# Optimization experiments

Hardware: AMD Instinct MI355X
Metric: run time of the kernel (lower is better)

The kernel has to match this reference:

```python
import jax, jax.numpy as jnp
import numpy as np
from jax import lax

T, B, E = 1500, 32, 512   # encoder frames, batch, encoded_size
H = 512                   # hidden_size
NC = 31                   # num_classes + 1 (EOS = 30)
LTXT = 100                # max text len before EOS column


def setup_inputs() -> dict:
    key = jax.random.key(0)
    ks = jax.random.split(key, 24)
    sE = 1.0 / np.sqrt(E); sH = 1.0 / np.sqrt(H); sIn = 1.0 / np.sqrt(H + E)
    inp = {
        'encoded': jax.random.normal(ks[0], (T, B, E), jnp.float32),
        'encoded_lens': jax.random.randint(ks[1], (B,), 1, T + 1),
        'texts': jax.random.randint(ks[2], (B, LTXT), 0, 30).astype(jnp.int32),
        'text_lens': jax.random.randint(ks[3], (B,), 1, LTXT + 1),
        # attention params
        'W_enc': jax.random.normal(ks[4], (H, E), jnp.float32) * sE,
        'b_enc': jax.random.normal(ks[5], (H,), jnp.float32) * sE,
        'W_rec': jax.random.normal(ks[6], (H, H), jnp.float32) * sH,
        'w_score': jax.random.normal(ks[7], (H,), jnp.float32) * sH,
        'b_score': jax.random.normal(ks[8], (), jnp.float32) * sH,
        # embedding
        'emb': jax.random.normal(ks[9], (NC, H), jnp.float32),
        # GRU layer 0 (input = H + E)
        'W_ih0': jax.random.normal(ks[10], (3 * H, H + E), jnp.float32) * sIn,
        'W_hh0': jax.random.normal(ks[11], (3 * H, H), jnp.float32) * sH,
        'b_ih0': jax.random.normal(ks[12], (3 * H,), jnp.float32) * sH,
        'b_hh0': jax.random.normal(ks[13], (3 * H,), jnp.float32) * sH,
        # GRU layer 1 (input = H)
        'W_ih1': jax.random.normal(ks[14], (3 * H, H), jnp.float32) * sH,
        'W_hh1': jax.random.normal(ks[15], (3 * H, H), jnp.float32) * sH,
        'b_ih1': jax.random.normal(ks[16], (3 * H,), jnp.float32) * sH,
        'b_hh1': jax.random.normal(ks[17], (3 * H,), jnp.float32) * sH,
        # output projection
        'W_out': jax.random.normal(ks[18], (NC, H), jnp.float32) * sH,
        'b_out': jax.random.normal(ks[19], (NC,), jnp.float32) * sH,
        # learned rnn zero state (n_layers, 1, H)
        'h0': jnp.zeros((2, 1, H), jnp.float32),
    }
    return inp


def _gru_cell(x, h, W_ih, W_hh, b_ih, b_hh):
    gi = x @ W_ih.T + b_ih
    gh = h @ W_hh.T + b_hh
    i_r, i_z, i_n = jnp.split(gi, 3, axis=-1)
    h_r, h_z, h_n = jnp.split(gh, 3, axis=-1)
    r = jax.nn.sigmoid(i_r + h_r)
    z = jax.nn.sigmoid(i_z + h_z)
    n = jnp.tanh(i_n + r * h_n)
    return (1.0 - z) * n + z * h


def reference(encoded, encoded_lens, texts, text_lens, W_enc, b_enc, W_rec,
              w_score, b_score, emb, W_ih0, W_hh0, b_ih0, b_hh0, W_ih1,
              W_hh1, b_ih1, b_hh1, W_out, b_out, h0):
    Tt, Bb, Ee = encoded.shape
    Hh = W_rec.shape[0]
    EOS = emb.shape[0] - 1
    # append zero column, then write EOS at text_lens position
    texts2 = jnp.concatenate([texts, jnp.zeros((Bb, 1), texts.dtype)], axis=1)
    texts2 = texts2.at[jnp.arange(Bb), text_lens].set(EOS)
    L = texts2.shape[1]
    embedded = emb[texts2.T]                               # (L, B, H)
    enc_contrib = encoded @ W_enc.T + b_enc                # (T, B, H)
    mask = (jnp.arange(Tt)[:, None] < encoded_lens[None, :]).astype(encoded.dtype)
    mask = (mask - 1.0) * 100000.0                         # (T, B)
    rnn0 = jnp.broadcast_to(h0, (2, Bb, Hh))

    def step(carry, target):
        rnn_state, inputs = carry
        rec = rnn_state[0] @ W_rec.T                       # (B, H)
        scores = jnp.tanh(enc_contrib + rec[None]) @ w_score + b_score  # (T, B)
        att = jax.nn.softmax(scores + mask, axis=0)        # (T, B)
        context = jnp.einsum('tb,tbe->be', att, encoded)   # (B, E)
        x = jnp.concatenate([inputs, context], axis=1)     # (B, H+E)
        h0n = _gru_cell(x, rnn_state[0], W_ih0, W_hh0, b_ih0, b_hh0)
        h1n = _gru_cell(h0n, rnn_state[1], W_ih1, W_hh1, b_ih1, b_hh1)
        return (jnp.stack([h0n, h1n]), target), h1n

    init = (rnn0, jnp.zeros((Bb, Hh), encoded.dtype))
    _, outputs = lax.scan(step, init, embedded)            # (L, B, H)
    logits = outputs @ W_out.T + b_out                     # (L, B, NC)
    logits = jnp.transpose(logits, (1, 0, 2)).reshape(Bb * L, -1)
    labels = texts2.reshape(-1)
    logp = jax.nn.log_softmax(logits, axis=-1)
    nll = -jnp.take_along_axis(logp, labels[:, None].astype(jnp.int32), axis=1)[:, 0]
    valid = (labels != 0).astype(logits.dtype)
    loss = jnp.sum(nll * valid) / jnp.maximum(jnp.sum(valid), 1.0)
    return loss
```

## Files before the change

kernel.cpp:

```cpp
#include <hip/hip_runtime.h>
#include <hip/hip_cooperative_groups.h>
#include <stdint.h>

#define T_FRAMES 1500
#define B_BATCH  32
#define E_DIM    512
#define H_DIM    512
#define NCLS     31
#define L_STEPS  101
#define EOS_TOK  30
#define NBLK     256
#define NTHR     1024
#define NSLICE   8

typedef unsigned short ushort_t;
typedef ushort_t ushort8_t __attribute__((ext_vector_type(8)));
typedef unsigned char uchar8_t __attribute__((ext_vector_type(8)));

__device__ __forceinline__ float bf2f(ushort_t u) {
    union { unsigned int i; float f; } v; v.i = ((unsigned int)u) << 16; return v.f;
}
__device__ __forceinline__ ushort_t f2bf(float f) {
    union { float f; unsigned int i; } v; v.f = f;
    unsigned int r = v.i + 0x7FFFu + ((v.i >> 16) & 1u);
    return (ushort_t)(r >> 16);
}
__device__ __forceinline__ float fp8tof(unsigned int u) {
    unsigned int e = (u >> 3) & 15u, m = u & 7u, sg = (u >> 7) & 1u;
    union { unsigned int i; float f; } v;
    v.i = (sg << 31) | ((e + 120u) << 23) | (m << 20);
    float sub = (float)(int)m * 0.001953125f;
    sub = sg ? -sub : sub;
    return e ? v.f : sub;
}
__device__ __forceinline__ unsigned char f2fp8(float x) {
    unsigned char sg = (x < 0.f) ? 0x80 : 0;
    float a = fabsf(x);
    if (!(a == a)) return (unsigned char)(sg | 0x7E);
    if (a >= 448.f) return (unsigned char)(sg | 0x7E);
    if (a < 0.015625f) {
        int m = (int)rintf(a * 512.f);
        if (m >= 8) return (unsigned char)(sg | 0x08);
        return (unsigned char)(sg | m);
    }
    union { float f; unsigned int i; } v; v.f = a;
    unsigned int r = v.i + 0x7FFFFu + ((v.i >> 20) & 1u);
    unsigned int e = (r >> 23) - 127u + 7u;
    unsigned int m = (r >> 20) & 7u;
    if (e > 15u || (e == 15u && m == 7u)) { e = 15u; m = 6u; }
    return (unsigned char)(sg | (e << 3) | m);
}
__device__ __forceinline__ float wave_sum(float v) {
    #pragma unroll
    for (int o = 32; o > 0; o >>= 1) v += __shfl_xor(v, o, 64);
    return v;
}
template<int N>
__device__ __forceinline__ void wave_sum_n(float* v) {
    #pragma unroll
    for (int o = 32; o > 0; o >>= 1) {
        #pragma unroll
        for (int i = 0; i < N; ++i) v[i] += __shfl_xor(v[i], o, 64);
    }
}
__device__ __forceinline__ float tanh_f(float x) {
    float e = __expf(2.0f * x);
    return 1.0f - 2.0f * __builtin_amdgcn_rcpf(e + 1.0f);
}
__device__ __forceinline__ float sigmoid_f(float x) {
    return __builtin_amdgcn_rcpf(1.0f + __expf(-x));
}

__device__ __forceinline__ float ld_byp(const float* p) {
    return __hip_atomic_load(p, __ATOMIC_RELAXED, __HIP_MEMORY_SCOPE_AGENT);
}
__device__ __forceinline__ void st_byp(float* p, float v) {
    __hip_atomic_store(p, v, __ATOMIC_RELAXED, __HIP_MEMORY_SCOPE_AGENT);
}

__device__ __forceinline__ void ffbarrier(int* flags, int base, int s, int k, int tid) {
    __syncthreads();
    if (tid == 0)
        __hip_atomic_store(&flags[(base + s) * 32], k,
                           __ATOMIC_RELAXED, __HIP_MEMORY_SCOPE_AGENT);
    if (tid < NSLICE) {
        while (__hip_atomic_load(&flags[(base + tid) * 32],
                                 __ATOMIC_RELAXED, __HIP_MEMORY_SCOPE_AGENT) < k)
            __builtin_amdgcn_s_sleep(1);
    }
    __syncthreads();
    asm volatile("" ::: "memory");
}

__global__ __launch_bounds__(256) void init_kernel(
    const int* __restrict__ texts, const int* __restrict__ text_lens,
    const float* __restrict__ h0p,
    int* __restrict__ texts2, float* __restrict__ h0buf, float* __restrict__ h1buf,
    float* __restrict__ acc, int* __restrict__ flags)
{
    int idx = blockIdx.x * 256 + threadIdx.x;
    if (idx < 2) acc[idx] = 0.f;
    if (idx < B_BATCH * NSLICE * 32) flags[idx] = 0;
    if (idx < B_BATCH * L_STEPS) {
        int b = idx / L_STEPS, j = idx % L_STEPS;
        int v = (j < 100) ? texts[b * 100 + j] : 0;
        if (j == text_lens[b]) v = EOS_TOK;
        texts2[idx] = v;
    }
    for (int i = idx; i < B_BATCH * H_DIM; i += gridDim.x * 256) {
        h0buf[i] = h0p[i & (H_DIM - 1)];
        h1buf[i] = h0p[H_DIM + (i & (H_DIM - 1))];
    }
}

__global__ __launch_bounds__(256) void cvt_kernel(const float* __restrict__ in,
                                                  ushort_t* __restrict__ out, int n) {
    int i = (blockIdx.x * 256 + threadIdx.x) * 8;
    if (i >= n) return;
    float4 a = *(const float4*)(in + i);
    float4 b = *(const float4*)(in + i + 4);
    ushort8_t o;
    o[0] = f2bf(a.x); o[1] = f2bf(a.y); o[2] = f2bf(a.z); o[3] = f2bf(a.w);
    o[4] = f2bf(b.x); o[5] = f2bf(b.y); o[6] = f2bf(b.z); o[7] = f2bf(b.w);
    *(ushort8_t*)(out + i) = o;
}

__global__ __launch_bounds__(64) void cvt_fp8_transpose_kernel(const float* __restrict__ in,
                                                               unsigned char* __restrict__ out) {
    int row = blockIdx.x;
    int t = row >> 5, b = row & 31;
    int k = threadIdx.x * 8;
    const float* ip = in + (size_t)row * E_DIM + k;
    float4 a = *(const float4*)(ip);
    float4 c = *(const float4*)(ip + 4);
    float vals[8] = {a.x, a.y, a.z, a.w, c.x, c.y, c.z, c.w};
    uchar8_t o;
    #pragma unroll
    for (int j = 0; j < 8; ++j) o[j] = f2fp8(vals[j]);
    *(uchar8_t*)(out + ((size_t)b * T_FRAMES + t) * E_DIM + k) = o;
}

#define GTM 128
#define GTN 128
#define GTK 32
#define GLDA (GTM + 4)

__global__ __launch_bounds__(256) void enc_gemm_kernel(
    const float* __restrict__ A, const float* __restrict__ W,
    const float* __restrict__ bias, ushort_t* __restrict__ C)
{
    __shared__ float As[GTK][GLDA];
    __shared__ float Bs[GTK][GLDA];
    const int m0 = blockIdx.y * GTM;
    const int n0 = blockIdx.x * GTN;
    const int tid = threadIdx.x;
    const int tx = tid & 15, ty = tid >> 4;
    const int lr = tid >> 3;
    const int lc = (tid & 7) << 2;
    float acc[8][8] = {};
    for (int k0 = 0; k0 < E_DIM; k0 += GTK) {
        #pragma unroll
        for (int p = 0; p < 4; ++p) {
            float4 a = *(const float4*)(A + (size_t)(m0 + lr + 32 * p) * E_DIM + k0 + lc);
            As[lc + 0][lr + 32 * p] = a.x; As[lc + 1][lr + 32 * p] = a.y;
            As[lc + 2][lr + 32 * p] = a.z; As[lc + 3][lr + 32 * p] = a.w;
            float4 b = *(const float4*)(W + (size_t)(n0 + lr + 32 * p) * E_DIM + k0 + lc);
            Bs[lc + 0][lr + 32 * p] = b.x; Bs[lc + 1][lr + 32 * p] = b.y;
            Bs[lc + 2][lr + 32 * p] = b.z; Bs[lc + 3][lr + 32 * p] = b.w;
        }
        __syncthreads();
        #pragma unroll
        for (int k = 0; k < GTK; ++k) {
            float av[8], bv[8];
            *(float4*)&av[0] = *(const float4*)&As[k][ty * 8];
            *(float4*)&av[4] = *(const float4*)&As[k][ty * 8 + 4];
            *(float4*)&bv[0] = *(const float4*)&Bs[k][tx * 8];
            *(float4*)&bv[4] = *(const float4*)&Bs[k][tx * 8 + 4];
            #pragma unroll
            for (int i = 0; i < 8; ++i)
                #pragma unroll
                for (int j = 0; j < 8; ++j)
                    acc[i][j] = fmaf(av[i], bv[j], acc[i][j]);
        }
        __syncthreads();
    }
    const float* bp = bias + n0 + tx * 8;
    #pragma unroll
    for (int i = 0; i < 8; ++i) {
        int m = m0 + ty * 8 + i;
        int b = m & 31, t = m >> 5;
        ushort8_t o;
        #pragma unroll
        for (int j = 0; j < 8; ++j) o[j] = f2bf(acc[i][j] + bp[j]);
        *(ushort8_t*)(C + ((size_t)b * T_FRAMES + t) * H_DIM + n0 + tx * 8) = o;
    }
}

struct Params {
    const float* encoded; const int* lens; const float* emb;
    const float* w_score; const float* b_score;
    const float* b_ih0; const float* b_hh0; const float* b_ih1; const float* b_hh1;
    const ushort_t* ec; const unsigned char* encF8;
    const ushort_t* Wrec; const ushort_t* Wih0; const ushort_t* Whh0;
    const ushort_t* Wih1; const ushort_t* Whh1;
    float* rec; float* ctxPart; float* denomPart;
    float* h0a; float* h0b; float* h1a; float* h1b;
    float* outputs; const int* texts2; int* flags;
    int useEncB;
};

__global__ __launch_bounds__(NTHR, 1) void decoder_kernel(Params p) {
    const int tid = threadIdx.x;
    const int bid = blockIdx.x;
    const int lane = tid & 63;
    const int wsub = tid >> 6;
    const int b = bid >> 3;
    const int s = bid & 7;
    const int fbase = b * NSLICE;
    __shared__ float sctx[16][E_DIM];
    __shared__ float sred[16];
    float* sA = &sctx[0][0];
    float* sB = &sctx[1][0];

    {
        const float* xp = p.h0a + b * H_DIM + lane * 8;
        float x8[8];
        *(float4*)&x8[0] = *(const float4*)(xp);
        *(float4*)&x8[4] = *(const float4*)(xp + 4);
        #pragma unroll
        for (int i = 0; i < 4; ++i) {
            int h = s * 64 + wsub * 4 + i;
            ushort8_t w8 = *(const ushort8_t*)(p.Wrec + (size_t)h * H_DIM + lane * 8);
            float v = 0.f;
            #pragma unroll
            for (int j = 0; j < 8; ++j) v = fmaf(x8[j], bf2f(w8[j]), v);
            v = wave_sum(v);
            if (lane == 0) st_byp(&p.rec[b * H_DIM + h], v);
        }
    }
    ffbarrier(p.flags, fbase, s, 1, tid);

    const int len = p.lens[b];
    for (int l = 0; l < L_STEPS; ++l) {
        float* h0cur = (l & 1) ? p.h0b : p.h0a;
        float* h0nxt = (l & 1) ? p.h0a : p.h0b;
        float* h1cur = (l & 1) ? p.h1b : p.h1a;
        float* h1nxt = (l & 1) ? p.h1a : p.h1b;

        {
            for (int i = tid; i < H_DIM; i += NTHR)
                sA[i] = ld_byp(&p.rec[b * H_DIM + i]);
            __syncthreads();
            float rec8[8], w8[8];
            #pragma unroll
            for (int j = 0; j < 8; ++j) rec8[j] = sA[lane * 8 + j];
            const float* wp = p.w_score + lane * 8;
            *(float4*)&w8[0] = *(const float4*)(wp);
            *(float4*)&w8[4] = *(const float4*)(wp + 4);
            float bsc = p.b_score[0];
            __syncthreads();
            float acc8[8] = {0.f,0.f,0.f,0.f,0.f,0.f,0.f,0.f};
            float dsum = 0.f;
            const int gw = wsub * NSLICE + s;
            if (p.useEncB) {
                const ushort_t* ecb = p.ec + (size_t)b * T_FRAMES * H_DIM + lane * 8;
                const unsigned char* efb = p.encF8 + (size_t)b * T_FRAMES * E_DIM + lane * 8;
                for (int t = gw; t < len; t += 256) {
                    int t2 = t + 128;
                    bool has2 = t2 < len;
                    int t2c = has2 ? t2 : t;
                    ushort8_t e8a = *(const ushort8_t*)(ecb + (size_t)t   * H_DIM);
                    ushort8_t e8b = *(const ushort8_t*)(ecb + (size_t)t2c * H_DIM);
                    uchar8_t v8a = *(const uchar8_t*)(efb + (size_t)t   * E_DIM);
                    uchar8_t v8b = *(const uchar8_t*)(efb + (size_t)t2c * E_DIM);
                    float ss[2] = {0.f, 0.f};
                    #pragma unroll
                    for (int j = 0; j < 8; ++j) {
                        ss[0] = fmaf(tanh_f(bf2f(e8a[j]) + rec8[j]), w8[j], ss[0]);
                        ss[1] = fmaf(tanh_f(bf2f(e8b[j]) + rec8[j]), w8[j], ss[1]);
                    }
                    wave_sum_n<2>(ss);
                    float pv0 = __expf(ss[0] + bsc);
                    float pv1 = has2 ? __expf(ss[1] + bsc) : 0.f;
                    dsum += pv0 + pv1;
                    #pragma unroll
                    for (int j = 0; j < 8; ++j)
                        acc8[j] += pv0 * fp8tof(v8a[j]) + pv1 * fp8tof(v8b[j]);
                }
            } else {
                const ushort_t* ecb = p.ec + (size_t)b * T_FRAMES * H_DIM + lane * 8;
                for (int t = gw; t < len; t += 128) {
                    ushort8_t e8 = *(const ushort8_t*)(ecb + (size_t)t * H_DIM);
                    float ss = 0.f;
                    #pragma unroll
                    for (int j = 0; j < 8; ++j)
                        ss = fmaf(tanh_f(bf2f(e8[j]) + rec8[j]), w8[j], ss);
                    ss = wave_sum(ss) + bsc;
                    float pv = __expf(ss);
                    dsum += pv;
                    const float* vp = p.encoded + ((size_t)t * B_BATCH + b) * E_DIM + lane * 8;
                    float v8[8];
                    *(float4*)&v8[0] = *(const float4*)(vp);
                    *(float4*)&v8[4] = *(const float4*)(vp + 4);
                    #pragma unroll
                    for (int j = 0; j < 8; ++j)
                        acc8[j] = fmaf(pv, v8[j], acc8[j]);
                }
            }
            *(float4*)&sctx[wsub][lane * 8]     = *(float4*)&acc8[0];
            *(float4*)&sctx[wsub][lane * 8 + 4] = *(float4*)&acc8[4];
            if (lane == 0) sred[wsub] = dsum;
            __syncthreads();
            if (tid < E_DIM) {
                float csum = 0.f;
                #pragma unroll
                for (int w = 0; w < 16; ++w) csum += sctx[w][tid];
                st_byp(&p.ctxPart[((size_t)b * NSLICE + s) * E_DIM + tid], csum);
            }
            if (tid == 0) {
                float d = 0.f;
                #pragma unroll
                for (int w = 0; w < 16; ++w) d += sred[w];
                st_byp(&p.denomPart[b * NSLICE + s], d);
            }
        }
        ffbarrier(p.flags, fbase, s, 3 * l + 2, tid);

        {
            if (tid < E_DIM) {
                float c = 0.f;
                #pragma unroll
                for (int s2 = 0; s2 < NSLICE; ++s2)
                    c += ld_byp(&p.ctxPart[((size_t)b * NSLICE + s2) * E_DIM + tid]);
                sA[tid] = c;
                sB[tid] = ld_byp(&h0cur[b * H_DIM + tid]);
            } else if (tid < E_DIM + NSLICE) {
                sred[tid - E_DIM] = ld_byp(&p.denomPart[b * NSLICE + (tid - E_DIM)]);
            }
            __syncthreads();
            float den = sred[0] + sred[1] + sred[2] + sred[3]
                      + sred[4] + sred[5] + sred[6] + sred[7];
            float inv = __builtin_amdgcn_rcpf(den);
            int token = (l > 0) ? p.texts2[b * L_STEPS + l - 1] : -1;
            float x16[16];
            int k0 = lane * 16;
            if (k0 < H_DIM) {
                if (token >= 0) {
                    const float* ep = p.emb + (size_t)token * H_DIM + k0;
                    #pragma unroll
                    for (int q = 0; q < 4; ++q)
                        *(float4*)&x16[q * 4] = *(const float4*)(ep + q * 4);
                } else {
                    #pragma unroll
                    for (int j = 0; j < 16; ++j) x16[j] = 0.f;
                }
            } else {
                #pragma unroll
                for (int j = 0; j < 16; ++j) x16[j] = sA[k0 - H_DIM + j] * inv;
            }
            float h8[8];
            #pragma unroll
            for (int j = 0; j < 8; ++j) h8[j] = sB[lane * 8 + j];
            const int IN = H_DIM + E_DIM;
            #pragma unroll
            for (int i = 0; i < 4; ++i) {
                int h = s * 64 + wsub * 4 + i;
                float v[6] = {0.f,0.f,0.f,0.f,0.f,0.f};
                #pragma unroll
                for (int g = 0; g < 3; ++g) {
                    const ushort_t* r = p.Wih0 + (size_t)(g * H_DIM + h) * IN + k0;
                    ushort8_t a = *(const ushort8_t*)(r);
                    ushort8_t c = *(const ushort8_t*)(r + 8);
                    #pragma unroll
                    for (int j = 0; j < 8; ++j) {
                        v[g] = fmaf(x16[j], bf2f(a[j]), v[g]);
                        v[g] = fmaf(x16[8 + j], bf2f(c[j]), v[g]);
                    }
                }
                #pragma unroll
                for (int g = 0; g < 3; ++g) {
                    const ushort_t* r = p.Whh0 + (size_t)(g * H_DIM + h) * H_DIM + lane * 8;
                    ushort8_t a = *(const ushort8_t*)(r);
                    #pragma unroll
                    for (int j = 0; j < 8; ++j)
                        v[3 + g] = fmaf(h8[j], bf2f(a[j]), v[3 + g]);
                }
                wave_sum_n<6>(v);
                if (lane == 0) {
                    float r = sigmoid_f(v[0] + p.b_ih0[h] + v[3] + p.b_hh0[h]);
                    float z = sigmoid_f(v[1] + p.b_ih0[H_DIM + h] + v[4] + p.b_hh0[H_DIM + h]);
                    float n = tanh_f(v[2] + p.b_ih0[2 * H_DIM + h] + r * (v[5] + p.b_hh0[2 * H_DIM + h]));
                    float hv = sB[h];
                    st_byp(&h0nxt[b * H_DIM + h], (1.f - z) * n + z * hv);
                }
            }
        }
        ffbarrier(p.flags, fbase, s, 3 * l + 3, tid);

        {
            if (tid < E_DIM) {
                sA[tid] = ld_byp(&h0nxt[b * H_DIM + tid]);
                sB[tid] = ld_byp(&h1cur[b * H_DIM + tid]);
            }
            __syncthreads();
            float x8[8], g8[8];
            #pragma unroll
            for (int j = 0; j < 8; ++j) { x8[j] = sA[lane * 8 + j]; g8[j] = sB[lane * 8 + j]; }
            #pragma unroll
            for (int i = 0; i < 4; ++i) {
                int h = s * 64 + wsub * 4 + i;
                float v[7] = {0.f,0.f,0.f,0.f,0.f,0.f,0.f};
                #pragma unroll
                for (int g = 0; g < 3; ++g) {
                    const ushort_t* r1 = p.Wih1 + (size_t)(g * H_DIM + h) * H_DIM + lane * 8;
                    ushort8_t a = *(const ushort8_t*)(r1);
                    const ushort_t* r2 = p.Whh1 + (size_t)(g * H_DIM + h) * H_DIM + lane * 8;
                    ushort8_t c = *(const ushort8_t*)(r2);
                    #pragma unroll
                    for (int j = 0; j < 8; ++j) {
                        v[g]     = fmaf(x8[j], bf2f(a[j]), v[g]);
                        v[3 + g] = fmaf(g8[j], bf2f(c[j]), v[3 + g]);
                    }
                }
                {
                    const ushort_t* r = p.Wrec + (size_t)h * H_DIM + lane * 8;
                    ushort8_t a = *(const ushort8_t*)(r);
                    #pragma unroll
                    for (int j = 0; j < 8; ++j)
                        v[6] = fmaf(x8[j], bf2f(a[j]), v[6]);
                }
                wave_sum_n<7>(v);
                if (lane == 0) {
                    float r = sigmoid_f(v[0] + p.b_ih1[h] + v[3] + p.b_hh1[h]);
                    float z = sigmoid_f(v[1] + p.b_ih1[H_DIM + h] + v[4] + p.b_hh1[H_DIM + h]);
                    float n = tanh_f(v[2] + p.b_ih1[2 * H_DIM + h] + r * (v[5] + p.b_hh1[2 * H_DIM + h]));
                    float hv = sB[h];
                    float out = (1.f - z) * n + z * hv;
                    st_byp(&h1nxt[b * H_DIM + h], out);
                    p.outputs[((size_t)l * B_BATCH + b) * H_DIM + h] = out;
                    st_byp(&p.rec[b * H_DIM + h], v[6]);
                }
            }
        }
        ffbarrier(p.flags, fbase, s, 3 * l + 4, tid);
    }
}

__global__ __launch_bounds__(256) void loss_kernel(
    const float* __restrict__ outputs, const int* __restrict__ texts2,
    const float* __restrict__ W_out, const float* __restrict__ b_out,
    float* __restrict__ acc)
{
    int wid = threadIdx.x >> 6, lane = threadIdx.x & 63;
    int gw = blockIdx.x * 4 + wid;
    int nw = gridDim.x * 4;
    float lsum = 0.f, lcnt = 0.f;
    for (int r = gw; r < B_BATCH * L_STEPS; r += nw) {
        int b = r / L_STEPS, l = r % L_STEPS;
        int label = texts2[r];
        const float* orow = outputs + ((size_t)l * B_BATCH + b) * H_DIM;
        int k = lane * 8;
        float o8[8];
        *(float4*)&o8[0] = *(const float4*)(orow + k);
        *(float4*)&o8[4] = *(const float4*)(orow + k + 4);
        float m = -1e30f, se = 0.f, ll = 0.f;
        for (int c = 0; c < NCLS; ++c) {
            const float* wrow = W_out + (size_t)c * H_DIM + k;
            float p = 0.f;
            #pragma unroll
            for (int j = 0; j < 8; ++j) p = fmaf(o8[j], wrow[j], p);
            float logit = wave_sum(p) + b_out[c];
            if (c == label) ll = logit;
            if (logit > m) { se = se * expf(m - logit) + 1.f; m = logit; }
            else           { se += expf(logit - m); }
        }
        float lse = m + logf(se);
        if (label != 0) { lsum += lse - ll; lcnt += 1.f; }
    }
    if (lane == 0) { atomicAdd(&acc[0], lsum); atomicAdd(&acc[1], lcnt); }
}

__global__ void finalize_kernel(const float* __restrict__ acc, float* __restrict__ out) {
    out[0] = acc[0] / fmaxf(acc[1], 1.0f);
}

static inline size_t align256(size_t x) { return (x + 255) & ~(size_t)255; }

extern "C" void kernel_launch(void* const* d_in, const int* in_sizes, int n_in,
                              void* d_out, int out_size, void* d_ws, size_t ws_size,
                              hipStream_t stream) {
    (void)in_sizes; (void)n_in; (void)out_size;
    const float* encoded      = (const float*)d_in[0];
    const int*   encoded_lens = (const int*)d_in[1];
    const int*   texts        = (const int*)d_in[2];
    const int*   text_lens    = (const int*)d_in[3];
    const float* W_enc        = (const float*)d_in[4];
    const float* b_enc        = (const float*)d_in[5];
    const float* W_rec        = (const float*)d_in[6];
    const float* w_score      = (const float*)d_in[7];
    const float* b_score      = (const float*)d_in[8];
    const float* emb          = (const float*)d_in[9];
    const float* W_ih0        = (const float*)d_in[10];
    const float* W_hh0        = (const float*)d_in[11];
    const float* b_ih0        = (const float*)d_in[12];
    const float* b_hh0        = (const float*)d_in[13];
    const float* W_ih1        = (const float*)d_in[14];
    const float* W_hh1        = (const float*)d_in[15];
    const float* b_ih1        = (const float*)d_in[16];
    const float* b_hh1        = (const float*)d_in[17];
    const float* W_out        = (const float*)d_in[18];
    const float* b_out        = (const float*)d_in[19];
    const float* h0p          = (const float*)d_in[20];

    char* ws = (char*)d_ws;
    size_t off = 0;
    ushort_t* ec     = (ushort_t*)(ws + off); off = align256(off + (size_t)T_FRAMES * B_BATCH * H_DIM * 2);
    ushort_t* Wrecb  = (ushort_t*)(ws + off); off = align256(off + (size_t)H_DIM * H_DIM * 2);
    ushort_t* Wih0b  = (ushort_t*)(ws + off); off = align256(off + (size_t)3 * H_DIM * (H_DIM + E_DIM) * 2);
    ushort_t* Whh0b  = (ushort_t*)(ws + off); off = align256(off + (size_t)3 * H_DIM * H_DIM * 2);
    ushort_t* Wih1b  = (ushort_t*)(ws + off); off = align256(off + (size_t)3 * H_DIM * H_DIM * 2);
    ushort_t* Whh1b  = (ushort_t*)(ws + off); off = align256(off + (size_t)3 * H_DIM * H_DIM * 2);
    float* rec       = (float*)(ws + off); off = align256(off + (size_t)B_BATCH * H_DIM * 4);
    float* ctxPart   = (float*)(ws + off); off = align256(off + (size_t)B_BATCH * NSLICE * E_DIM * 4);
    float* denomPart = (float*)(ws + off); off = align256(off + (size_t)B_BATCH * NSLICE * 4);
    float* h0a       = (float*)(ws + off); off = align256(off + (size_t)B_BATCH * H_DIM * 4);
    float* h0b       = (float*)(ws + off); off = align256(off + (size_t)B_BATCH * H_DIM * 4);
    float* h1a       = (float*)(ws + off); off = align256(off + (size_t)B_BATCH * H_DIM * 4);
    float* h1b       = (float*)(ws + off); off = align256(off + (size_t)B_BATCH * H_DIM * 4);
    float* outputs   = (float*)(ws + off); off = align256(off + (size_t)L_STEPS * B_BATCH * H_DIM * 4);
    int*   texts2    = (int*)(ws + off); off = align256(off + (size_t)B_BATCH * L_STEPS * 4);
    float* acc       = (float*)(ws + off); off = align256(off + 256);
    int*   flags     = (int*)(ws + off); off = align256(off + (size_t)B_BATCH * NSLICE * 32 * 4);
    size_t encF8_off = off;
    size_t encF8_bytes = (size_t)T_FRAMES * B_BATCH * E_DIM;
    int useEncB = (encF8_off + encF8_bytes <= ws_size) ? 1 : 0;
    unsigned char* encF8 = (unsigned char*)(ws + encF8_off);

    init_kernel<<<64, 256, 0, stream>>>(texts, text_lens, h0p, texts2, h0a, h1a, acc, flags);
    cvt_kernel<<<(H_DIM * H_DIM) / (256 * 8), 256, 0, stream>>>(W_rec, Wrecb, H_DIM * H_DIM);
    cvt_kernel<<<(3 * H_DIM * (H_DIM + E_DIM)) / (256 * 8), 256, 0, stream>>>(W_ih0, Wih0b, 3 * H_DIM * (H_DIM + E_DIM));
    cvt_kernel<<<(3 * H_DIM * H_DIM) / (256 * 8), 256, 0, stream>>>(W_hh0, Whh0b, 3 * H_DIM * H_DIM);
    cvt_kernel<<<(3 * H_DIM * H_DIM) / (256 * 8), 256, 0, stream>>>(W_ih1, Wih1b, 3 * H_DIM * H_DIM);
    cvt_kernel<<<(3 * H_DIM * H_DIM) / (256 * 8), 256, 0, stream>>>(W_hh1, Whh1b, 3 * H_DIM * H_DIM);
    if (useEncB) {
        cvt_fp8_transpose_kernel<<<T_FRAMES * B_BATCH, 64, 0, stream>>>(encoded, encF8);
    }
    enc_gemm_kernel<<<dim3(H_DIM / GTN, (T_FRAMES * B_BATCH) / GTM), 256, 0, stream>>>(
        encoded, W_enc, b_enc, ec);

    Params prm;
    prm.encoded = encoded; prm.lens = encoded_lens; prm.emb = emb;
    prm.w_score = w_score; prm.b_score = b_score;
    prm.b_ih0 = b_ih0; prm.b_hh0 = b_hh0; prm.b_ih1 = b_ih1; prm.b_hh1 = b_hh1;
    prm.ec = ec; prm.encF8 = encF8;
    prm.Wrec = Wrecb; prm.Wih0 = Wih0b; prm.Whh0 = Whh0b; prm.Wih1 = Wih1b; prm.Whh1 = Whh1b;
    prm.rec = rec; prm.ctxPart = ctxPart; prm.denomPart = denomPart;
    prm.h0a = h0a; prm.h0b = h0b; prm.h1a = h1a; prm.h1b = h1b;
    prm.outputs = outputs; prm.texts2 = texts2; prm.flags = flags;
    prm.useEncB = useEncB;

    void* args[] = { &prm };
    hipLaunchCooperativeKernel((const void*)decoder_kernel, dim3(NBLK), dim3(NTHR),
                               args, 0, stream);

    loss_kernel<<<64, 256, 0, stream>>>(outputs, texts2, W_out, b_out, acc);
    finalize_kernel<<<1, 1, 0, stream>>>(acc, (float*)d_out);
}
```

Measured before the change: 8.736 ms.

## Interleave fp8 enc-projection and values into fused layout; double decoder blocks

Stores the encoder projection in fp8 instead of bf16 and interleaves it with the fp8 encoded values into one 1024-byte row per frame. Each lane now does a single 16-byte load that covers both the score and context operands. The decoder grid doubles to 512 blocks with 16 slices per batch, so each block handles half the hidden rows and a smaller stride of frames. This halves the traffic of the per-step attention scan but adds fp8 rounding error to the scores. It also relies on the cooperative launch fitting 512 blocks of 1024 threads, with launch bounds raised to 8.

```diff
diff --git a/kernel.cpp b/kernel.cpp
--- a/kernel.cpp
+++ b/kernel.cpp
@@ -9,13 +9,14 @@
 #define NCLS     31
 #define L_STEPS  101
 #define EOS_TOK  30
-#define NBLK     256
+#define NBLK     512
 #define NTHR     1024
-#define NSLICE   8
+#define NSLICE   16
 
 typedef unsigned short ushort_t;
 typedef ushort_t ushort8_t __attribute__((ext_vector_type(8)));
 typedef unsigned char uchar8_t __attribute__((ext_vector_type(8)));
+typedef unsigned char uchar16_t __attribute__((ext_vector_type(16)));
 
 __device__ __forceinline__ float bf2f(ushort_t u) {
     union { unsigned int i; float f; } v; v.i = ((unsigned int)u) << 16; return v.f;
@@ -125,8 +126,8 @@
     *(ushort8_t*)(out + i) = o;
 }
 
-__global__ __launch_bounds__(64) void cvt_fp8_transpose_kernel(const float* __restrict__ in,
-                                                               unsigned char* __restrict__ out) {
+__global__ __launch_bounds__(64) void cvt_fused_enc_kernel(const float* __restrict__ in,
+                                                           unsigned char* __restrict__ fused) {
     int row = blockIdx.x;
     int t = row >> 5, b = row & 31;
     int k = threadIdx.x * 8;
@@ -137,7 +138,7 @@
     uchar8_t o;
     #pragma unroll
     for (int j = 0; j < 8; ++j) o[j] = f2fp8(vals[j]);
-    *(uchar8_t*)(out + ((size_t)b * T_FRAMES + t) * E_DIM + k) = o;
+    *(uchar8_t*)(fused + ((size_t)b * T_FRAMES + t) * 1024 + threadIdx.x * 16 + 8) = o;
 }
 
 #define GTM 128
@@ -147,7 +148,7 @@
 
 __global__ __launch_bounds__(256) void enc_gemm_kernel(
     const float* __restrict__ A, const float* __restrict__ W,
-    const float* __restrict__ bias, ushort_t* __restrict__ C)
+    const float* __restrict__ bias, unsigned char* __restrict__ fused)
 {
     __shared__ float As[GTK][GLDA];
     __shared__ float Bs[GTK][GLDA];
@@ -189,33 +190,32 @@
     for (int i = 0; i < 8; ++i) {
         int m = m0 + ty * 8 + i;
         int b = m & 31, t = m >> 5;
-        ushort8_t o;
+        uchar8_t o;
         #pragma unroll
-        for (int j = 0; j < 8; ++j) o[j] = f2bf(acc[i][j] + bp[j]);
-        *(ushort8_t*)(C + ((size_t)b * T_FRAMES + t) * H_DIM + n0 + tx * 8) = o;
+        for (int j = 0; j < 8; ++j) o[j] = f2fp8(acc[i][j] + bp[j]);
+        *(uchar8_t*)(fused + ((size_t)b * T_FRAMES + t) * 1024 + ((n0 + tx * 8) >> 3) * 16) = o;
     }
 }
 
 struct Params {
-    const float* encoded; const int* lens; const float* emb;
+    const int* lens; const float* emb;
     const float* w_score; const float* b_score;
     const float* b_ih0; const float* b_hh0; const float* b_ih1; const float* b_hh1;
-    const ushort_t* ec; const unsigned char* encF8;
+    const unsigned char* fused;
     const ushort_t* Wrec; const ushort_t* Wih0; const ushort_t* Whh0;
     const ushort_t* Wih1; const ushort_t* Whh1;
     float* rec; float* ctxPart; float* denomPart;
     float* h0a; float* h0b; float* h1a; float* h1b;
     float* outputs; const int* texts2; int* flags;
-    int useEncB;
 };
 
-__global__ __launch_bounds__(NTHR, 1) void decoder_kernel(Params p) {
+__global__ __launch_bounds__(NTHR, 8) void decoder_kernel(Params p) {
     const int tid = threadIdx.x;
     const int bid = blockIdx.x;
     const int lane = tid & 63;
     const int wsub = tid >> 6;
-    const int b = bid >> 3;
-    const int s = bid & 7;
+    const int b = bid >> 4;
+    const int s = bid & 15;
     const int fbase = b * NSLICE;
     __shared__ float sctx[16][E_DIM];
     __shared__ float sred[16];
@@ -228,8 +228,8 @@
         *(float4*)&x8[0] = *(const float4*)(xp);
         *(float4*)&x8[4] = *(const float4*)(xp + 4);
         #pragma unroll
-        for (int i = 0; i < 4; ++i) {
-            int h = s * 64 + wsub * 4 + i;
+        for (int i = 0; i < 2; ++i) {
+            int h = s * 32 + wsub * 2 + i;
             ushort8_t w8 = *(const ushort8_t*)(p.Wrec + (size_t)h * H_DIM + lane * 8);
             float v = 0.f;
             #pragma unroll
@@ -262,50 +262,26 @@
             float acc8[8] = {0.f,0.f,0.f,0.f,0.f,0.f,0.f,0.f};
             float dsum = 0.f;
             const int gw = wsub * NSLICE + s;
-            if (p.useEncB) {
-                const ushort_t* ecb = p.ec + (size_t)b * T_FRAMES * H_DIM + lane * 8;
-                const unsigned char* efb = p.encF8 + (size_t)b * T_FRAMES * E_DIM + lane * 8;
-                for (int t = gw; t < len; t += 256) {
-                    int t2 = t + 128;
-                    bool has2 = t2 < len;
-                    int t2c = has2 ? t2 : t;
-                    ushort8_t e8a = *(const ushort8_t*)(ecb + (size_t)t   * H_DIM);
-                    ushort8_t e8b = *(const ushort8_t*)(ecb + (size_t)t2c * H_DIM);
-                    uchar8_t v8a = *(const uchar8_t*)(efb + (size_t)t   * E_DIM);
-                    uchar8_t v8b = *(const uchar8_t*)(efb + (size_t)t2c * E_DIM);
-                    float ss[2] = {0.f, 0.f};
-                    #pragma unroll
-                    for (int j = 0; j < 8; ++j) {
-                        ss[0] = fmaf(tanh_f(bf2f(e8a[j]) + rec8[j]), w8[j], ss[0]);
-                        ss[1] = fmaf(tanh_f(bf2f(e8b[j]) + rec8[j]), w8[j], ss[1]);
-                    }
-                    wave_sum_n<2>(ss);
-                    float pv0 = __expf(ss[0] + bsc);
-                    float pv1 = has2 ? __expf(ss[1] + bsc) : 0.f;
-                    dsum += pv0 + pv1;
-                    #pragma unroll
-                    for (int j = 0; j < 8; ++j)
-                        acc8[j] += pv0 * fp8tof(v8a[j]) + pv1 * fp8tof(v8b[j]);
-                }
-            } else {
-                const ushort_t* ecb = p.ec + (size_t)b * T_FRAMES * H_DIM + lane * 8;
-                for (int t = gw; t < len; t += 128) {
-                    ushort8_t e8 = *(const ushort8_t*)(ecb + (size_t)t * H_DIM);
-                    float ss = 0.f;
-                    #pragma unroll
-                    for (int j = 0; j < 8; ++j)
-                        ss = fmaf(tanh_f(bf2f(e8[j]) + rec8[j]), w8[j], ss);
-                    ss = wave_sum(ss) + bsc;
-                    float pv = __expf(ss);
-                    dsum += pv;
-                    const float* vp = p.encoded + ((size_t)t * B_BATCH + b) * E_DIM + lane * 8;
-                    float v8[8];
-                    *(float4*)&v8[0] = *(const float4*)(vp);
-                    *(float4*)&v8[4] = *(const float4*)(vp + 4);
-                    #pragma unroll
-                    for (int j = 0; j < 8; ++j)
-                        acc8[j] = fmaf(pv, v8[j], acc8[j]);
-                }
+            const unsigned char* fb = p.fused + (size_t)b * T_FRAMES * 1024 + lane * 16;
+            for (int t = gw; t < len; t += 512) {
+                int t2 = t + 256;
+                bool has2 = t2 < len;
+                int t2c = has2 ? t2 : t;
+                uchar16_t ua = *(const uchar16_t*)(fb + (size_t)t   * 1024);
+                uchar16_t ub = *(const uchar16_t*)(fb + (size_t)t2c * 1024);
+                float ss[2] = {0.f, 0.f};
+                #pragma unroll
+                for (int j = 0; j < 8; ++j) {
+                    ss[0] = fmaf(tanh_f(fp8tof(ua[j]) + rec8[j]), w8[j], ss[0]);
+                    ss[1] = fmaf(tanh_f(fp8tof(ub[j]) + rec8[j]), w8[j], ss[1]);
+                }
+                wave_sum_n<2>(ss);
+                float pv0 = __expf(ss[0] + bsc);
+                float pv1 = has2 ? __expf(ss[1] + bsc) : 0.f;
+                dsum += pv0 + pv1;
+                #pragma unroll
+                for (int j = 0; j < 8; ++j)
+                    acc8[j] += pv0 * fp8tof(ua[8 + j]) + pv1 * fp8tof(ub[8 + j]);
             }
             *(float4*)&sctx[wsub][lane * 8]     = *(float4*)&acc8[0];
             *(float4*)&sctx[wsub][lane * 8 + 4] = *(float4*)&acc8[4];
@@ -338,8 +314,9 @@
                 sred[tid - E_DIM] = ld_byp(&p.denomPart[b * NSLICE + (tid - E_DIM)]);
             }
             __syncthreads();
-            float den = sred[0] + sred[1] + sred[2] + sred[3]
-                      + sred[4] + sred[5] + sred[6] + sred[7];
+            float den = 0.f;
+            #pragma unroll
+            for (int s2 = 0; s2 < NSLICE; ++s2) den += sred[s2];
             float inv = __builtin_amdgcn_rcpf(den);
             int token = (l > 0) ? p.texts2[b * L_STEPS + l - 1] : -1;
             float x16[16];
@@ -363,8 +340,8 @@
             for (int j = 0; j < 8; ++j) h8[j] = sB[lane * 8 + j];
             const int IN = H_DIM + E_DIM;
             #pragma unroll
-            for (int i = 0; i < 4; ++i) {
-                int h = s * 64 + wsub * 4 + i;
+            for (int i = 0; i < 2; ++i) {
+                int h = s * 32 + wsub * 2 + i;
                 float v[6] = {0.f,0.f,0.f,0.f,0.f,0.f};
                 #pragma unroll
                 for (int g = 0; g < 3; ++g) {
@@ -407,8 +384,8 @@
             #pragma unroll
             for (int j = 0; j < 8; ++j) { x8[j] = sA[lane * 8 + j]; g8[j] = sB[lane * 8 + j]; }
             #pragma unroll
-            for (int i = 0; i < 4; ++i) {
-                int h = s * 64 + wsub * 4 + i;
+            for (int i = 0; i < 2; ++i) {
+                int h = s * 32 + wsub * 2 + i;
                 float v[7] = {0.f,0.f,0.f,0.f,0.f,0.f,0.f};
                 #pragma unroll
                 for (int g = 0; g < 3; ++g) {
@@ -489,7 +466,7 @@
 extern "C" void kernel_launch(void* const* d_in, const int* in_sizes, int n_in,
                               void* d_out, int out_size, void* d_ws, size_t ws_size,
                               hipStream_t stream) {
-    (void)in_sizes; (void)n_in; (void)out_size;
+    (void)in_sizes; (void)n_in; (void)out_size; (void)ws_size;
     const float* encoded      = (const float*)d_in[0];
     const int*   encoded_lens = (const int*)d_in[1];
     const int*   texts        = (const int*)d_in[2];
@@ -514,7 +491,7 @@
 
     char* ws = (char*)d_ws;
     size_t off = 0;
-    ushort_t* ec     = (ushort_t*)(ws + off); off = align256(off + (size_t)T_FRAMES * B_BATCH * H_DIM * 2);
+    unsigned char* fused = (unsigned char*)(ws + off); off = align256(off + (size_t)T_FRAMES * B_BATCH * 1024);
     ushort_t* Wrecb  = (ushort_t*)(ws + off); off = align256(off + (size_t)H_DIM * H_DIM * 2);
     ushort_t* Wih0b  = (ushort_t*)(ws + off); off = align256(off + (size_t)3 * H_DIM * (H_DIM + E_DIM) * 2);
     ushort_t* Whh0b  = (ushort_t*)(ws + off); off = align256(off + (size_t)3 * H_DIM * H_DIM * 2);
@@ -531,10 +508,6 @@
     int*   texts2    = (int*)(ws + off); off = align256(off + (size_t)B_BATCH * L_STEPS * 4);
     float* acc       = (float*)(ws + off); off = align256(off + 256);
     int*   flags     = (int*)(ws + off); off = align256(off + (size_t)B_BATCH * NSLICE * 32 * 4);
-    size_t encF8_off = off;
-    size_t encF8_bytes = (size_t)T_FRAMES * B_BATCH * E_DIM;
-    int useEncB = (encF8_off + encF8_bytes <= ws_size) ? 1 : 0;
-    unsigned char* encF8 = (unsigned char*)(ws + encF8_off);
 
     init_kernel<<<64, 256, 0, stream>>>(texts, text_lens, h0p, texts2, h0a, h1a, acc, flags);
     cvt_kernel<<<(H_DIM * H_DIM) / (256 * 8), 256, 0, stream>>>(W_rec, Wrecb, H_DIM * H_DIM);
@@ -542,22 +515,19 @@
     cvt_kernel<<<(3 * H_DIM * H_DIM) / (256 * 8), 256, 0, stream>>>(W_hh0, Whh0b, 3 * H_DIM * H_DIM);
     cvt_kernel<<<(3 * H_DIM * H_DIM) / (256 * 8), 256, 0, stream>>>(W_ih1, Wih1b, 3 * H_DIM * H_DIM);
     cvt_kernel<<<(3 * H_DIM * H_DIM) / (256 * 8), 256, 0, stream>>>(W_hh1, Whh1b, 3 * H_DIM * H_DIM);
-    if (useEncB) {
-        cvt_fp8_transpose_kernel<<<T_FRAMES * B_BATCH, 64, 0, stream>>>(encoded, encF8);
-    }
+    cvt_fused_enc_kernel<<<T_FRAMES * B_BATCH, 64, 0, stream>>>(encoded, fused);
     enc_gemm_kernel<<<dim3(H_DIM / GTN, (T_FRAMES * B_BATCH) / GTM), 256, 0, stream>>>(
-        encoded, W_enc, b_enc, ec);
+        encoded, W_enc, b_enc, fused);
 
     Params prm;
-    prm.encoded = encoded; prm.lens = encoded_lens; prm.emb = emb;
+    prm.lens = encoded_lens; prm.emb = emb;
     prm.w_score = w_score; prm.b_score = b_score;
     prm.b_ih0 = b_ih0; prm.b_hh0 = b_hh0; prm.b_ih1 = b_ih1; prm.b_hh1 = b_hh1;
-    prm.ec = ec; prm.encF8 = encF8;
+    prm.fused = fused;
     prm.Wrec = Wrecb; prm.Wih0 = Wih0b; prm.Whh0 = Whh0b; prm.Wih1 = Wih1b; prm.Whh1 = Whh1b;
     prm.rec = rec; prm.ctxPart = ctxPart; prm.denomPart = denomPart;
     prm.h0a = h0a; prm.h0b = h0b; prm.h1a = h1a; prm.h1b = h1b;
     prm.outputs = outputs; prm.texts2 = texts2; prm.flags = flags;
-    prm.useEncB = useEncB;
 
     void* args[] = { &prm };
     hipLaunchCooperativeKernel((const void*)decoder_kernel, dim3(NBLK), dim3(NTHR),
```

Result: slower. 12.42 ms (+42.2%).
